# Optimization experiments

Measured on AMD Instinct MI355X. Metric: run time of the kernel, lower is better.

The kernel has to match this reference:

```python
import jax, jax.numpy as jnp
import numpy as np

DIM = 256
HEADS = 8
HEAD_DIM = DIM // HEADS
B = 8
HH, WW = 32, 32
N = HH * WW
TABLE = (2 * HH - 1) * (2 * WW - 1)  # 3969
CPB_HID = 512


def _l2norm(t, eps=1e-12):
    # matches torch F.normalize(dim=-1): x / max(||x||, eps)
    n = jnp.sqrt(jnp.sum(t * t, axis=-1, keepdims=True))
    return t / jnp.maximum(n, eps)


def setup_inputs() -> dict:
    key = jax.random.key(0)
    ks = jax.random.split(key, 12)
    x = jax.random.normal(ks[0], (B, N, DIM), dtype=jnp.float32)
    relative_pos_index = jax.random.randint(ks[1], (N, N), 0, TABLE)
    relative_coords_table = jax.random.normal(ks[2], (TABLE, 2), dtype=jnp.float32)
    s = 0.02
    qkv_w = jax.random.normal(ks[3], (3 * DIM, DIM), dtype=jnp.float32) * s
    qkv_b = jnp.zeros((3 * DIM,), dtype=jnp.float32)
    query_embedding = jax.random.normal(ks[4], (HEADS, 1, HEAD_DIM), dtype=jnp.float32) * s
    # temperature init: log(exp(1/0.24) - 1) so softplus(temperature) = 1/0.24
    temperature = jnp.full((HEADS, 1, 1), float(np.log(np.expm1(1.0 / 0.24))), dtype=jnp.float32)
    proj_w = jax.random.normal(ks[5], (DIM, DIM), dtype=jnp.float32) * s
    proj_b = jnp.zeros((DIM,), dtype=jnp.float32)
    cpb_fc1_w = jax.random.normal(ks[6], (CPB_HID, 2), dtype=jnp.float32) * s
    cpb_fc1_b = jnp.zeros((CPB_HID,), dtype=jnp.float32)
    cpb_fc2_w = jax.random.normal(ks[7], (HEADS, CPB_HID), dtype=jnp.float32) * s
    cpb_fc2_b = jnp.zeros((HEADS,), dtype=jnp.float32)
    return dict(x=x, H=HH, W=WW, relative_pos_index=relative_pos_index,
                relative_coords_table=relative_coords_table,
                qkv_w=qkv_w, qkv_b=qkv_b, query_embedding=query_embedding,
                temperature=temperature, proj_w=proj_w, proj_b=proj_b,
                cpb_fc1_w=cpb_fc1_w, cpb_fc1_b=cpb_fc1_b,
                cpb_fc2_w=cpb_fc2_w, cpb_fc2_b=cpb_fc2_b)


def reference(x, H, W, relative_pos_index, relative_coords_table,
              qkv_w, qkv_b, query_embedding, temperature,
              proj_w, proj_b, cpb_fc1_w, cpb_fc1_b, cpb_fc2_w, cpb_fc2_b):
    Bc, Nc, C = x.shape
    seq_length_scale = jnp.asarray(np.log(HH * WW), dtype=x.dtype)  # from init input_resolution
    # qkv projection -> [B, heads, N, head_dim] each
    qkv = (x @ qkv_w.T + qkv_b).reshape(Bc, Nc, 3 * HEADS, HEAD_DIM).transpose(0, 2, 1, 3)
    q, k, v = qkv[:, :HEADS], qkv[:, HEADS:2 * HEADS], qkv[:, 2 * HEADS:]
    # CPB relative position bias: small MLP over coord table, then NxN gather
    h = jax.nn.relu(relative_coords_table @ cpb_fc1_w.T + cpb_fc1_b)  # [T, 512]
    table = (h @ cpb_fc2_w.T + cpb_fc2_b).T                           # [heads, T]
    rel_bias = table[:, relative_pos_index.reshape(-1)].reshape(HEADS, Nc, Nc)
    # cosine attention with learned temperature
    qn = _l2norm(q) + query_embedding[None]                           # [B, heads, N, hd]
    scale = jax.nn.softplus(temperature) * seq_length_scale           # [heads, 1, 1]
    attn = jnp.einsum('bhnd,bhmd->bhnm', qn * scale[None], _l2norm(k)) + rel_bias[None]
    attn = jax.nn.softmax(attn, axis=-1)
    out = jnp.einsum('bhnm,bhmd->bhnd', attn, v).transpose(0, 2, 1, 3).reshape(Bc, Nc, C)
    return out @ proj_w.T + proj_b
```

## Files before the change

### kernel.cpp

```cpp
#include <hip/hip_runtime.h>
#include <hip/hip_bf16.h>
#include <cstddef>
#include <cstdint>

typedef float v4f __attribute__((ext_vector_type(4)));
typedef short v8s __attribute__((ext_vector_type(8)));
typedef _Float16 v8h __attribute__((ext_vector_type(8)));

__device__ __forceinline__ uint32_t fbits(float x){ uint32_t u; __builtin_memcpy(&u,&x,4); return u; }
__device__ __forceinline__ float ffrom(uint32_t u){ float f; __builtin_memcpy(&f,&u,4); return f; }
__device__ __forceinline__ short bf_rh(float x){ return (short)((fbits(x)+0x8000u)>>16); }
__device__ __forceinline__ uint32_t pack_bf_rh(float a, float b){
    uint32_t ua = fbits(a)+0x8000u, ub = fbits(b)+0x8000u;
#if __has_builtin(__builtin_amdgcn_perm)
    return __builtin_amdgcn_perm(ub, ua, 0x07060302u);
#else
    return (ua>>16) | (ub & 0xFFFF0000u);
#endif
}
__device__ __forceinline__ short f2h(float x){ _Float16 h = (_Float16)x; short s; __builtin_memcpy(&s,&h,2); return s; }
#if __has_builtin(__builtin_amdgcn_exp2f)
#define EXP2(x) __builtin_amdgcn_exp2f(x)
#else
#define EXP2(x) exp2f(x)
#endif

__device__ __forceinline__ void gld16(const void* g, void* l) {
    __builtin_amdgcn_global_load_lds(
        (const __attribute__((address_space(1))) unsigned int*)g,
        (__attribute__((address_space(3))) unsigned int*)l, 16, 0, 0);
}
#define MFMA(a,b,c)  __builtin_amdgcn_mfma_f32_16x16x32_bf16((a),(b),(c),0,0,0)
#define MFMAH(a,b,c) __builtin_amdgcn_mfma_f32_16x16x32_f16((a),(b),(c),0,0,0)

#define LOG2E 1.4426950408889634f

__global__ __launch_bounds__(256)
void fused_qkv(const float* __restrict__ x,   const float* __restrict__ wq,
               const float* __restrict__ wp,  const float* __restrict__ rct,
               const float* __restrict__ fc1w, const float* __restrict__ fc1b,
               const float* __restrict__ fc2w, const float* __restrict__ fc2b,
               const float* __restrict__ qkvb, const float* __restrict__ qe,
               const float* __restrict__ temp, const int* __restrict__ rpi,
               short* __restrict__ qh, short* __restrict__ kh,
               short* __restrict__ vt, float* __restrict__ tblf,
               short* __restrict__ wph, unsigned long long* __restrict__ bi)
{
    __shared__ __align__(16) char smem[49152];
    int bid  = blockIdx.x;
    int tid  = threadIdx.x;
    int w    = tid >> 6;
    int lane = tid & 63;
    int t    = lane & 15;
    int quad = lane >> 4;
    int lr8  = lane >> 3, lc8 = lane & 7;

    if (bid < 63) {
        float* s1 = (float*)smem;
        float* sb = s1 + 1024;
        float* s2 = sb + 512;
        for (int i = tid; i < 1024; i += 256) s1[i] = fc1w[i];
        for (int i = tid; i < 512;  i += 256) sb[i] = fc1b[i];
        for (int i = tid; i < 4096; i += 256) s2[i] = fc2w[i];
        __syncthreads();
        int rl = tid >> 2, jp = tid & 3;
        bool ok = rl < 63;
        int r = bid * 63 + rl;
        float c0 = ok ? rct[2*r]   : 0.f;
        float c1 = ok ? rct[2*r+1] : 0.f;
        float a[8] = {0,0,0,0,0,0,0,0};
        int j0 = jp * 128;
        #pragma unroll 4
        for (int j = j0; j < j0 + 128; ++j) {
            float hv = fmaxf(c0*s1[2*j] + c1*s1[2*j+1] + sb[j], 0.0f);
            #pragma unroll
            for (int hh = 0; hh < 8; ++hh) a[hh] += hv * s2[hh*512 + j];
        }
        #pragma unroll
        for (int hh = 0; hh < 8; ++hh) {
            a[hh] += __shfl_xor(a[hh], 1);
            a[hh] += __shfl_xor(a[hh], 2);
        }
        if (ok && jp == 0) {
            #pragma unroll
            for (int hh = 0; hh < 8; ++hh)
                tblf[hh*3969 + r] = (a[hh] + fc2b[hh]) * LOG2E;
        }
    } else if (bid < 95) {
        int base8 = (bid - 63) * 256;
        int e0 = (base8 + tid) * 8;
        int m  = e0 >> 8;
        int k  = e0 & 255;
        int kt = k >> 6, c = (k >> 3) & 7;
        float4 f0 = *(const float4*)(wp + e0);
        float4 f1 = *(const float4*)(wp + e0 + 4);
        float v[8] = {f0.x,f0.y,f0.z,f0.w,f1.x,f1.y,f1.z,f1.w};
        v8s hi;
        #pragma unroll
        for (int j = 0; j < 8; ++j) hi[j] = f2h(v[j]);
        int dst = m*256 + kt*64 + ((c ^ (m & 7)) << 3);
        *(v8s*)&wph[dst] = hi;
    } else if (bid < 159) {
        int q16 = bid - 95;
        int grp = tid >> 6;
        #pragma unroll 1
        for (int c = 0; c < 16; ++c) {
            int combo = grp*16 + c;
            int kt = combo >> 2, g = combo & 3;
            unsigned long long pk = 0;
            #pragma unroll
            for (int r = 0; r < 4; ++r) {
                int idx = rpi[(size_t)(q16*16 + quad*4 + r)*1024 + kt*64 + 4*t + g];
                pk |= (unsigned long long)(idx & 0xFFFF) << (16*r);
            }
            bi[((size_t)(q16*16 + kt)*4 + g)*64 + lane] = pk;
        }
    } else {
        short* A0 = (short*)smem;
        short* A1 = A0 + 128*64;
        short* W0 = A1 + 128*64;
        short* W1 = W0 + 64*64;
        int g2 = bid - 159;
        int n0 = (g2 % 12) * 64, m0 = (g2 / 12) * 128;
        int Mw = (w >> 1) * 64, Nw = (w & 1) * 32;

        v4f acc[4][2];
        #pragma unroll
        for (int mt = 0; mt < 4; ++mt)
            #pragma unroll
            for (int nt = 0; nt < 2; ++nt) acc[mt][nt] = (v4f){0,0,0,0};

        #pragma unroll 1
        for (int kt2 = 0; kt2 < 2; ++kt2) {
            __syncthreads();
            #pragma unroll
            for (int half = 0; half < 2; ++half) {
                int kt = kt2*2 + half;
                short* Ad = half ? A1 : A0;
                short* Wd = half ? W1 : W0;
                #pragma unroll
                for (int i = 0; i < 4; ++i) {
                    int rr = w*32 + i*8 + lr8;
                    const float* s = x + (size_t)(m0 + rr)*256 + kt*64 + lc8*8;
                    float4 f0 = *(const float4*)s;
                    float4 f1 = *(const float4*)(s + 4);
                    v8h hv;
                    hv[0]=(_Float16)f0.x; hv[1]=(_Float16)f0.y;
                    hv[2]=(_Float16)f0.z; hv[3]=(_Float16)f0.w;
                    hv[4]=(_Float16)f1.x; hv[5]=(_Float16)f1.y;
                    hv[6]=(_Float16)f1.z; hv[7]=(_Float16)f1.w;
                    *(v8h*)&Ad[rr*64 + ((lc8 ^ lr8) << 3)] = hv;
                }
                #pragma unroll
                for (int i = 0; i < 2; ++i) {
                    int rr = w*16 + i*8 + lr8;
                    const float* s = wq + (size_t)(n0 + rr)*256 + kt*64 + lc8*8;
                    float4 f0 = *(const float4*)s;
                    float4 f1 = *(const float4*)(s + 4);
                    v8h hv;
                    hv[0]=(_Float16)f0.x; hv[1]=(_Float16)f0.y;
                    hv[2]=(_Float16)f0.z; hv[3]=(_Float16)f0.w;
                    hv[4]=(_Float16)f1.x; hv[5]=(_Float16)f1.y;
                    hv[6]=(_Float16)f1.z; hv[7]=(_Float16)f1.w;
                    *(v8h*)&Wd[rr*64 + ((lc8 ^ lr8) << 3)] = hv;
                }
            }
            __syncthreads();
            #pragma unroll
            for (int half = 0; half < 2; ++half) {
                const short* As = half ? A1 : A0;
                const short* Ws = half ? W1 : W0;
                #pragma unroll
                for (int kk = 0; kk < 2; ++kk) {
                    int cp = ((kk*4 + quad) ^ (t & 7)) << 3;
                    v8h bh8[2];
                    #pragma unroll
                    for (int nt = 0; nt < 2; ++nt)
                        bh8[nt] = *(const v8h*)&Ws[(Nw + nt*16 + t)*64 + cp];
                    #pragma unroll
                    for (int mt = 0; mt < 4; ++mt) {
                        v8h ah = *(const v8h*)&As[(Mw + mt*16 + t)*64 + cp];
                        #pragma unroll
                        for (int nt = 0; nt < 2; ++nt)
                            acc[mt][nt] = MFMAH(ah, bh8[nt], acc[mt][nt]);
                    }
                }
            }
        }

        #pragma unroll
        for (int nt = 0; nt < 2; ++nt) {
            float bv = qkvb[n0 + Nw + nt*16 + t];
            #pragma unroll
            for (int mt = 0; mt < 4; ++mt)
                #pragma unroll
                for (int r = 0; r < 4; ++r) acc[mt][nt][r] += bv;
        }

        int which = n0 >> 8;
        if (which < 2) {
            int head = ((n0 + Nw) >> 5) & 7;
            float scale = 0.f;
            if (which == 0)
                scale = log1pf(__expf(temp[head])) * 10.0f;
            #pragma unroll
            for (int mt = 0; mt < 4; ++mt)
                #pragma unroll
                for (int r = 0; r < 4; ++r) {
                    float a0 = acc[mt][0][r], a1 = acc[mt][1][r];
                    float s = a0*a0 + a1*a1;
                    s += __shfl_xor(s, 1); s += __shfl_xor(s, 2);
                    s += __shfl_xor(s, 4); s += __shfl_xor(s, 8);
                    float inv = 1.0f / fmaxf(sqrtf(s), 1e-12f);
                    int m = m0 + Mw + mt*16 + quad*4 + r;
                    int b = m >> 10, nrow = m & 1023;
                    if (which == 0) {
                        size_t rowoff = (((size_t)b*8 + head)*1024 + nrow) * 32;
                        #pragma unroll
                        for (int nt = 0; nt < 2; ++nt) {
                            int d = nt*16 + t;
                            float val = (acc[mt][nt][r] * inv + qe[head*32 + d]) * scale;
                            qh[rowoff + d] = f2h(val);
                        }
                    } else {
                        int kk = nrow & 63;
                        int pp = (kk & 3)*16 + (kk >> 2);
                        int prow = (nrow & ~63) | pp;
                        int swk = (kk >> 3) & 3;
                        size_t rowoff = (((size_t)b*8 + head)*1024 + prow) * 32;
                        #pragma unroll
                        for (int nt = 0; nt < 2; ++nt) {
                            int d = nt*16 + t;
                            int dpos = (((d >> 3) ^ swk) << 3) | (d & 7);
                            kh[rowoff + dpos] = f2h(acc[mt][nt][r] * inv);
                        }
                    }
                }
        } else {
            __syncthreads();
            short* VT = (short*)smem;
            #pragma unroll
            for (int mt = 0; mt < 4; ++mt)
                #pragma unroll
                for (int nt = 0; nt < 2; ++nt) {
                    int cl = Nw + nt*16 + t;
                    #pragma unroll
                    for (int r = 0; r < 4; ++r) {
                        int rl = Mw + mt*16 + quad*4 + r;
                        VT[cl*136 + rl] = bf_rh(acc[mt][nt][r]);
                    }
                }
            __syncthreads();
            int b = m0 >> 10;
            int keybase = m0 & 1023;
            int headbase = ((n0 - 512) >> 5) & 7;
            int cl = tid >> 2;
            int dim = cl & 31;
            int hd  = headbase + (cl >> 5);
            size_t obase = (((size_t)b*8 + hd)*32 + dim) * 1024 + keybase;
            #pragma unroll
            for (int pz = 0; pz < 4; ++pz) {
                int ci  = (tid & 3) * 4 + pz;
                int ktl = ci >> 3, c = ci & 7;
                v8s val = *(const v8s*)&VT[cl*136 + ktl*64 + c*8];
                *(v8s*)&vt[obase + ktl*64 + ((c ^ (dim & 7)) << 3)] = val;
            }
        }
    }
}

__global__ __launch_bounds__(512)
void attn_mfma(const short* __restrict__ qh, const short* __restrict__ kh,
               const short* __restrict__ vt,
               const unsigned long long* __restrict__ bi,
               const float* __restrict__ tblf,
               short* __restrict__ yh)
{
    __shared__ __align__(16) short Kh_s[2][2048];
    __shared__ __align__(16) short Vt_s[2][2048];
    __shared__ __align__(16) short Ps[8][16][68];
    __shared__ float tb[3972];

    int bh  = blockIdx.x & 63;
    int qt  = blockIdx.x >> 6;
    int h   = bh & 7;
    int b   = bh >> 3;
    int tid = threadIdx.x;
    int w    = tid >> 6;
    int lane = tid & 63;
    int t    = lane & 15;
    int quad = lane >> 4;

    for (int i = tid; i < 3969; i += 512) tb[i] = tblf[h*3969 + i];

    size_t qoff = ((size_t)bh*1024 + qt*128 + w*16 + t) * 32 + quad*8;
    v8h qf = *(const v8h*)(qh + qoff);

    v4f Oacc[2] = {{0,0,0,0},{0,0,0,0}};
    float lsum[4] = {0,0,0,0};

    size_t kgbase = (size_t)bh * 32768;
    const unsigned long long* bmb = bi + (size_t)(qt*8 + w)*4096 + lane;
    int qrow0 = qt*128 + w*16 + quad*4;
    int swzS = (quad ^ ((t >> 1) & 3)) << 3;
    int lr8 = lane >> 3, lc8 = lane & 7;

    if (w < 4)
        gld16(kh + kgbase + w*512 + lane*8, &Kh_s[0][w*512]);
    else
        gld16(vt + kgbase + (size_t)((w-4)*8 + lr8)*1024 + lc8*8, &Vt_s[0][(w-4)*512]);
    unsigned long long curb[4];
    #pragma unroll
    for (int g = 0; g < 4; ++g) curb[g] = bmb[g*64];

    #pragma unroll 1
    for (int kt = 0; kt < 16; ++kt) {
        int cur = kt & 1;
        __syncthreads();
        unsigned long long nxtb[4];
        if (kt < 15) {
            int nkt = kt + 1, nb = cur ^ 1;
            if (w < 4)
                gld16(kh + kgbase + (size_t)nkt*2048 + w*512 + lane*8, &Kh_s[nb][w*512]);
            else
                gld16(vt + kgbase + (size_t)((w-4)*8 + lr8)*1024 + nkt*64 + lc8*8,
                      &Vt_s[nb][(w-4)*512]);
            #pragma unroll
            for (int g = 0; g < 4; ++g) nxtb[g] = bmb[nkt*256 + g*64];
        }

        v4f S[4];
        #pragma unroll
        for (int g = 0; g < 4; ++g) {
            v8h kb = *(const v8h*)&Kh_s[cur][(g*16 + t)*32 + swzS];
            unsigned long long cb = curb[g];
            v4f c;
            c[0] = tb[(uint32_t)cb & 0xFFFFu];
            c[1] = tb[(uint32_t)(cb >> 16) & 0xFFFFu];
            c[2] = tb[(uint32_t)(cb >> 32) & 0xFFFFu];
            c[3] = tb[(uint32_t)(cb >> 48)];
            S[g] = MFMAH(qf, kb, c);
        }

        #pragma unroll
        for (int r = 0; r < 4; ++r) {
            float p0 = EXP2(S[0][r]);
            float p1 = EXP2(S[1][r]);
            float p2 = EXP2(S[2][r]);
            float p3 = EXP2(S[3][r]);
            lsum[r] += (p0 + p1) + (p2 + p3);
            uint2 pk;
            pk.x = pack_bf_rh(p0, p1);
            pk.y = pack_bf_rh(p2, p3);
            *(uint2*)&Ps[w][quad*4 + r][t*4] = pk;
        }

        #pragma unroll
        for (int ks = 0; ks < 2; ++ks) {
            v8s pf = *(const v8s*)&Ps[w][t][ks*32 + quad*8];
            int vsw = ((ks*4 + quad) ^ (t & 7)) << 3;
            #pragma unroll
            for (int g = 0; g < 2; ++g) {
                v8s vf = *(const v8s*)&Vt_s[cur][(g*16 + t)*64 + vsw];
                Oacc[g] = MFMA(pf, vf, Oacc[g]);
            }
        }
        #pragma unroll
        for (int g = 0; g < 4; ++g) curb[g] = nxtb[g];
    }

    #pragma unroll
    for (int r = 0; r < 4; ++r) {
        float l = lsum[r];
        l += __shfl_xor(l, 1); l += __shfl_xor(l, 2);
        l += __shfl_xor(l, 4); l += __shfl_xor(l, 8);
        float inv = 1.0f / l;
        int qrow = qrow0 + r;
        int m = b*1024 + qrow;
        size_t mbase = (size_t)m * 256;
        int mk = m & 7;
        #pragma unroll
        for (int g = 0; g < 2; ++g) {
            float o = Oacc[g][r] * inv;
            int c = h*4 + g*2 + (t >> 3);
            int chp = ((c ^ mk) << 3) | (t & 7);
            yh[mbase + chp] = f2h(o);
        }
    }
}

__global__ __launch_bounds__(256)
void gemm_proj(const short* __restrict__ Ah_g, const short* __restrict__ Wh_g,
               const float* __restrict__ bias, float* __restrict__ C, int N)
{
    __shared__ __align__(16) short As[2][4096];
    __shared__ __align__(16) short Ws[2][4096];

    int tid  = threadIdx.x;
    int w    = tid >> 6;
    int lane = tid & 63;
    int t    = lane & 15;
    int quad = lane >> 4;
    int m0 = blockIdx.y * 64, n0 = blockIdx.x * 64;
    int Mw = (w >> 1) * 32, Nw = (w & 1) * 32;

    v4f acc[2][2];
    #pragma unroll
    for (int mt = 0; mt < 2; ++mt)
        #pragma unroll
        for (int nt = 0; nt < 2; ++nt) acc[mt][nt] = (v4f){0,0,0,0};

    int lr8 = lane >> 3, lc8 = lane & 7;
    #pragma unroll 1
    for (int kt2 = 0; kt2 < 2; ++kt2) {
        __syncthreads();
        #pragma unroll
        for (int half = 0; half < 2; ++half) {
            int kt = kt2*2 + half;
            #pragma unroll
            for (int i = 0; i < 2; ++i) {
                size_t grow = (size_t)(m0 + w*16 + i*8 + lr8) * 256 + kt*64 + lc8*8;
                gld16(Ah_g + grow, &As[half][(w*16 + i*8) * 64]);
            }
            #pragma unroll
            for (int i = 0; i < 2; ++i) {
                size_t grow = (size_t)(n0 + w*16 + i*8 + lr8) * 256 + kt*64 + lc8*8;
                gld16(Wh_g + grow, &Ws[half][(w*16 + i*8) * 64]);
            }
        }
        __syncthreads();
        #pragma unroll
        for (int half = 0; half < 2; ++half) {
            #pragma unroll
            for (int kk = 0; kk < 2; ++kk) {
                int cp = ((kk*4 + quad) ^ (t & 7)) << 3;
                v8h bh8[2];
                #pragma unroll
                for (int nt = 0; nt < 2; ++nt)
                    bh8[nt] = *(const v8h*)&Ws[half][(Nw + nt*16 + t)*64 + cp];
                #pragma unroll
                for (int mt = 0; mt < 2; ++mt) {
                    v8h ah = *(const v8h*)&As[half][(Mw + mt*16 + t)*64 + cp];
                    #pragma unroll
                    for (int nt = 0; nt < 2; ++nt)
                        acc[mt][nt] = MFMAH(ah, bh8[nt], acc[mt][nt]);
                }
            }
        }
    }

    #pragma unroll
    for (int nt = 0; nt < 2; ++nt) {
        float bv = bias[n0 + Nw + nt*16 + t];
        #pragma unroll
        for (int mt = 0; mt < 2; ++mt)
            #pragma unroll
            for (int r = 0; r < 4; ++r) acc[mt][nt][r] += bv;
    }
    #pragma unroll
    for (int mt = 0; mt < 2; ++mt)
        #pragma unroll
        for (int r = 0; r < 4; ++r) {
            int m = m0 + Mw + mt*16 + quad*4 + r;
            #pragma unroll
            for (int nt = 0; nt < 2; ++nt)
                C[(size_t)m * N + n0 + Nw + nt*16 + t] = acc[mt][nt][r];
        }
}

extern "C" void kernel_launch(void* const* d_in, const int* in_sizes, int n_in,
                              void* d_out, int out_size, void* d_ws, size_t ws_size,
                              hipStream_t stream)
{
    const float* x     = (const float*)d_in[0];
    const int*   rpi   = (const int*)d_in[3];
    const float* rct   = (const float*)d_in[4];
    const float* qkvw  = (const float*)d_in[5];
    const float* qkvb  = (const float*)d_in[6];
    const float* qe    = (const float*)d_in[7];
    const float* temp  = (const float*)d_in[8];
    const float* projw = (const float*)d_in[9];
    const float* projb = (const float*)d_in[10];
    const float* fc1w  = (const float*)d_in[11];
    const float* fc1b  = (const float*)d_in[12];
    const float* fc2w  = (const float*)d_in[13];
    const float* fc2b  = (const float*)d_in[14];

    char* p = (char*)d_ws;
    float* tblf  = (float*)p;  p += 131072;
    short* y     = (short*)p;  p += 4194304;
    short* wph   = (short*)p;  p += 131072;
    short* qh    = (short*)p;  p += 4194304;
    short* kh    = (short*)p;  p += 4194304;
    short* vt    = (short*)p;  p += 4194304;
    unsigned long long* bi = (unsigned long long*)p; p += 2097152;
    float* out   = (float*)d_out;

    fused_qkv<<<927, 256, 0, stream>>>(x, qkvw, projw, rct,
                                       fc1w, fc1b, fc2w, fc2b,
                                       qkvb, qe, temp, rpi,
                                       qh, kh, vt, tblf, wph, bi);

    attn_mfma<<<512, 512, 0, stream>>>(qh, kh, vt, bi, tblf, y);

    dim3 g2(256/64, 8192/64);
    gemm_proj<<<g2, 256, 0, stream>>>(y, wph, projb, out, 256);
}
```

Baseline: 148.4 us.

## Fuse output projection into attention kernel via last-arriving-block atomic counter

Removes the separate projection GEMM launch. Blocks are reordered so that the eight heads sharing a (batch, query-tile) row group increment a per-group atomic counter. The last block to finish then runs the 128x256 projection for that group from the fp16 attention output, using the shared memory that attention already used. This saves a kernel launch and its tail, but the projection is serialized onto one block per group, which lowers its parallelism and adds fences and atomics. The counters are reset inside the first kernel.

```diff
diff --git a/kernel.cpp b/kernel.cpp
--- a/kernel.cpp
+++ b/kernel.cpp
@@ -44,7 +44,8 @@
                const float* __restrict__ temp, const int* __restrict__ rpi,
                short* __restrict__ qh, short* __restrict__ kh,
                short* __restrict__ vt, float* __restrict__ tblf,
-               short* __restrict__ wph, unsigned long long* __restrict__ bi)
+               short* __restrict__ wph, unsigned long long* __restrict__ bi,
+               unsigned* __restrict__ done)
 {
     __shared__ __align__(16) char smem[49152];
     int bid  = blockIdx.x;
@@ -102,6 +103,7 @@
         *(v8s*)&wph[dst] = hi;
     } else if (bid < 159) {
         int q16 = bid - 95;
+        if (q16 == 0 && tid < 64) done[tid] = 0;
         int grp = tid >> 6;
         #pragma unroll 1
         for (int c = 0; c < 16; ++c) {
@@ -274,22 +276,30 @@
                const short* __restrict__ vt,
                const unsigned long long* __restrict__ bi,
                const float* __restrict__ tblf,
-               short* __restrict__ yh)
+               short* __restrict__ yh,
+               const short* __restrict__ wph,
+               const float* __restrict__ projb,
+               float* __restrict__ out,
+               unsigned* __restrict__ done)
 {
-    __shared__ __align__(16) short Kh_s[2][2048];
-    __shared__ __align__(16) short Vt_s[2][2048];
-    __shared__ __align__(16) short Ps[8][16][68];
-    __shared__ float tb[3972];
-
-    int bh  = blockIdx.x & 63;
-    int qt  = blockIdx.x >> 6;
-    int h   = bh & 7;
-    int b   = bh >> 3;
+    __shared__ __align__(16) char smem[49696];
+    __shared__ unsigned wflag;
+    short* Kh  = (short*)smem;
+    short* Vts = Kh + 4096;
+    short* Psb = Vts + 4096;
+    float* tb  = (float*)(Psb + 8704);
+
+    int h   = blockIdx.x >> 6;
+    int g   = blockIdx.x & 63;
+    int b   = g >> 3;
+    int qt  = g & 7;
+    int bh  = b*8 + h;
     int tid = threadIdx.x;
     int w    = tid >> 6;
     int lane = tid & 63;
     int t    = lane & 15;
     int quad = lane >> 4;
+    int lr8 = lane >> 3, lc8 = lane & 7;
 
     for (int i = tid; i < 3969; i += 512) tb[i] = tblf[h*3969 + i];
 
@@ -303,15 +313,14 @@
     const unsigned long long* bmb = bi + (size_t)(qt*8 + w)*4096 + lane;
     int qrow0 = qt*128 + w*16 + quad*4;
     int swzS = (quad ^ ((t >> 1) & 3)) << 3;
-    int lr8 = lane >> 3, lc8 = lane & 7;
 
     if (w < 4)
-        gld16(kh + kgbase + w*512 + lane*8, &Kh_s[0][w*512]);
+        gld16(kh + kgbase + w*512 + lane*8, &Kh[w*512]);
     else
-        gld16(vt + kgbase + (size_t)((w-4)*8 + lr8)*1024 + lc8*8, &Vt_s[0][(w-4)*512]);
+        gld16(vt + kgbase + (size_t)((w-4)*8 + lr8)*1024 + lc8*8, &Vts[(w-4)*512]);
     unsigned long long curb[4];
     #pragma unroll
-    for (int g = 0; g < 4; ++g) curb[g] = bmb[g*64];
+    for (int gg = 0; gg < 4; ++gg) curb[gg] = bmb[gg*64];
 
     #pragma unroll 1
     for (int kt = 0; kt < 16; ++kt) {
@@ -321,25 +330,26 @@
         if (kt < 15) {
             int nkt = kt + 1, nb = cur ^ 1;
             if (w < 4)
-                gld16(kh + kgbase + (size_t)nkt*2048 + w*512 + lane*8, &Kh_s[nb][w*512]);
+                gld16(kh + kgbase + (size_t)nkt*2048 + w*512 + lane*8,
+                      &Kh[nb*2048 + w*512]);
             else
                 gld16(vt + kgbase + (size_t)((w-4)*8 + lr8)*1024 + nkt*64 + lc8*8,
-                      &Vt_s[nb][(w-4)*512]);
-            #pragma unroll
-            for (int g = 0; g < 4; ++g) nxtb[g] = bmb[nkt*256 + g*64];
+                      &Vts[nb*2048 + (w-4)*512]);
+            #pragma unroll
+            for (int gg = 0; gg < 4; ++gg) nxtb[gg] = bmb[nkt*256 + gg*64];
         }
 
         v4f S[4];
         #pragma unroll
-        for (int g = 0; g < 4; ++g) {
-            v8h kb = *(const v8h*)&Kh_s[cur][(g*16 + t)*32 + swzS];
-            unsigned long long cb = curb[g];
+        for (int gg = 0; gg < 4; ++gg) {
+            v8h kb = *(const v8h*)&Kh[cur*2048 + (gg*16 + t)*32 + swzS];
+            unsigned long long cb = curb[gg];
             v4f c;
             c[0] = tb[(uint32_t)cb & 0xFFFFu];
             c[1] = tb[(uint32_t)(cb >> 16) & 0xFFFFu];
             c[2] = tb[(uint32_t)(cb >> 32) & 0xFFFFu];
             c[3] = tb[(uint32_t)(cb >> 48)];
-            S[g] = MFMAH(qf, kb, c);
+            S[gg] = MFMAH(qf, kb, c);
         }
 
         #pragma unroll
@@ -352,21 +362,21 @@
             uint2 pk;
             pk.x = pack_bf_rh(p0, p1);
             pk.y = pack_bf_rh(p2, p3);
-            *(uint2*)&Ps[w][quad*4 + r][t*4] = pk;
+            *(uint2*)&Psb[(w*16 + quad*4 + r)*68 + t*4] = pk;
         }
 
         #pragma unroll
         for (int ks = 0; ks < 2; ++ks) {
-            v8s pf = *(const v8s*)&Ps[w][t][ks*32 + quad*8];
+            v8s pf = *(const v8s*)&Psb[(w*16 + t)*68 + ks*32 + quad*8];
             int vsw = ((ks*4 + quad) ^ (t & 7)) << 3;
             #pragma unroll
-            for (int g = 0; g < 2; ++g) {
-                v8s vf = *(const v8s*)&Vt_s[cur][(g*16 + t)*64 + vsw];
-                Oacc[g] = MFMA(pf, vf, Oacc[g]);
-            }
-        }
-        #pragma unroll
-        for (int g = 0; g < 4; ++g) curb[g] = nxtb[g];
+            for (int gg = 0; gg < 2; ++gg) {
+                v8s vf = *(const v8s*)&Vts[cur*2048 + (gg*16 + t)*64 + vsw];
+                Oacc[gg] = MFMA(pf, vf, Oacc[gg]);
+            }
+        }
+        #pragma unroll
+        for (int gg = 0; gg < 4; ++gg) curb[gg] = nxtb[gg];
     }
 
     #pragma unroll
@@ -380,92 +390,93 @@
         size_t mbase = (size_t)m * 256;
         int mk = m & 7;
         #pragma unroll
-        for (int g = 0; g < 2; ++g) {
-            float o = Oacc[g][r] * inv;
-            int c = h*4 + g*2 + (t >> 3);
+        for (int gg = 0; gg < 2; ++gg) {
+            float o = Oacc[gg][r] * inv;
+            int c = h*4 + gg*2 + (t >> 3);
             int chp = ((c ^ mk) << 3) | (t & 7);
             yh[mbase + chp] = f2h(o);
         }
     }
-}
-
-__global__ __launch_bounds__(256)
-void gemm_proj(const short* __restrict__ Ah_g, const short* __restrict__ Wh_g,
-               const float* __restrict__ bias, float* __restrict__ C, int N)
-{
-    __shared__ __align__(16) short As[2][4096];
-    __shared__ __align__(16) short Ws[2][4096];
-
-    int tid  = threadIdx.x;
-    int w    = tid >> 6;
-    int lane = tid & 63;
-    int t    = lane & 15;
-    int quad = lane >> 4;
-    int m0 = blockIdx.y * 64, n0 = blockIdx.x * 64;
-    int Mw = (w >> 1) * 32, Nw = (w & 1) * 32;
-
-    v4f acc[2][2];
-    #pragma unroll
-    for (int mt = 0; mt < 2; ++mt)
-        #pragma unroll
-        for (int nt = 0; nt < 2; ++nt) acc[mt][nt] = (v4f){0,0,0,0};
-
-    int lr8 = lane >> 3, lc8 = lane & 7;
+
+    __threadfence();
+    __syncthreads();
+    if (tid == 0) {
+        unsigned prev = __hip_atomic_fetch_add(&done[g], 1u,
+                            __ATOMIC_ACQ_REL, __HIP_MEMORY_SCOPE_AGENT);
+        wflag = (prev == 7u);
+    }
+    __syncthreads();
+    if (!wflag) return;
+    __threadfence();
+    __syncthreads();
+
+    int m0g = b*1024 + qt*128;
+    int grp = w >> 2;
+    int wl  = w & 3;
+    short* Asg = (short*)smem + grp*8192;
+    short* Wsg = Asg + 4096;
+    int Mw = (wl >> 1) * 32, Nw = (wl & 1) * 32;
+
     #pragma unroll 1
-    for (int kt2 = 0; kt2 < 2; ++kt2) {
-        __syncthreads();
-        #pragma unroll
-        for (int half = 0; half < 2; ++half) {
-            int kt = kt2*2 + half;
+    for (int vbp = 0; vbp < 4; ++vbp) {
+        int v = vbp*2 + grp;
+        int m0v = m0g + (v >> 2) * 64;
+        int n0v = (v & 3) * 64;
+        v4f pacc[2][2];
+        #pragma unroll
+        for (int mt = 0; mt < 2; ++mt)
+            #pragma unroll
+            for (int nt = 0; nt < 2; ++nt) pacc[mt][nt] = (v4f){0,0,0,0};
+
+        #pragma unroll 1
+        for (int kt3 = 0; kt3 < 4; ++kt3) {
+            __syncthreads();
             #pragma unroll
             for (int i = 0; i < 2; ++i) {
-                size_t grow = (size_t)(m0 + w*16 + i*8 + lr8) * 256 + kt*64 + lc8*8;
-                gld16(Ah_g + grow, &As[half][(w*16 + i*8) * 64]);
+                int rr = wl*16 + i*8 + lr8;
+                gld16(yh + (size_t)(m0v + rr)*256 + kt3*64 + lc8*8, Asg + rr*64);
             }
             #pragma unroll
             for (int i = 0; i < 2; ++i) {
-                size_t grow = (size_t)(n0 + w*16 + i*8 + lr8) * 256 + kt*64 + lc8*8;
-                gld16(Wh_g + grow, &Ws[half][(w*16 + i*8) * 64]);
-            }
-        }
-        __syncthreads();
-        #pragma unroll
-        for (int half = 0; half < 2; ++half) {
+                int rr = wl*16 + i*8 + lr8;
+                gld16(wph + (size_t)(n0v + rr)*256 + kt3*64 + lc8*8, Wsg + rr*64);
+            }
+            __syncthreads();
             #pragma unroll
             for (int kk = 0; kk < 2; ++kk) {
                 int cp = ((kk*4 + quad) ^ (t & 7)) << 3;
                 v8h bh8[2];
                 #pragma unroll
                 for (int nt = 0; nt < 2; ++nt)
-                    bh8[nt] = *(const v8h*)&Ws[half][(Nw + nt*16 + t)*64 + cp];
+                    bh8[nt] = *(const v8h*)&Wsg[(Nw + nt*16 + t)*64 + cp];
                 #pragma unroll
                 for (int mt = 0; mt < 2; ++mt) {
-                    v8h ah = *(const v8h*)&As[half][(Mw + mt*16 + t)*64 + cp];
+                    v8h ah = *(const v8h*)&Asg[(Mw + mt*16 + t)*64 + cp];
                     #pragma unroll
                     for (int nt = 0; nt < 2; ++nt)
-                        acc[mt][nt] = MFMAH(ah, bh8[nt], acc[mt][nt]);
+                        pacc[mt][nt] = MFMAH(ah, bh8[nt], pacc[mt][nt]);
                 }
             }
         }
+
+        #pragma unroll
+        for (int nt = 0; nt < 2; ++nt) {
+            float bv = projb[n0v + Nw + nt*16 + t];
+            #pragma unroll
+            for (int mt = 0; mt < 2; ++mt)
+                #pragma unroll
+                for (int r = 0; r < 4; ++r) pacc[mt][nt][r] += bv;
+        }
+        #pragma unroll
+        for (int mt = 0; mt < 2; ++mt)
+            #pragma unroll
+            for (int r = 0; r < 4; ++r) {
+                int m = m0v + Mw + mt*16 + quad*4 + r;
+                #pragma unroll
+                for (int nt = 0; nt < 2; ++nt)
+                    out[(size_t)m * 256 + n0v + Nw + nt*16 + t] = pacc[mt][nt][r];
+            }
     }
-
-    #pragma unroll
-    for (int nt = 0; nt < 2; ++nt) {
-        float bv = bias[n0 + Nw + nt*16 + t];
-        #pragma unroll
-        for (int mt = 0; mt < 2; ++mt)
-            #pragma unroll
-            for (int r = 0; r < 4; ++r) acc[mt][nt][r] += bv;
-    }
-    #pragma unroll
-    for (int mt = 0; mt < 2; ++mt)
-        #pragma unroll
-        for (int r = 0; r < 4; ++r) {
-            int m = m0 + Mw + mt*16 + quad*4 + r;
-            #pragma unroll
-            for (int nt = 0; nt < 2; ++nt)
-                C[(size_t)m * N + n0 + Nw + nt*16 + t] = acc[mt][nt][r];
-        }
 }
 
 extern "C" void kernel_launch(void* const* d_in, const int* in_sizes, int n_in,
@@ -494,15 +505,14 @@
     short* kh    = (short*)p;  p += 4194304;
     short* vt    = (short*)p;  p += 4194304;
     unsigned long long* bi = (unsigned long long*)p; p += 2097152;
+    unsigned* done = (unsigned*)p; p += 256;
     float* out   = (float*)d_out;
 
     fused_qkv<<<927, 256, 0, stream>>>(x, qkvw, projw, rct,
                                        fc1w, fc1b, fc2w, fc2b,
                                        qkvb, qe, temp, rpi,
-                                       qh, kh, vt, tblf, wph, bi);
-
-    attn_mfma<<<512, 512, 0, stream>>>(qh, kh, vt, bi, tblf, y);
-
-    dim3 g2(256/64, 8192/64);
-    gemm_proj<<<g2, 256, 0, stream>>>(y, wph, projb, out, 256);
+                                       qh, kh, vt, tblf, wph, bi, done);
+
+    attn_mfma<<<512, 512, 0, stream>>>(qh, kh, vt, bi, tblf, y,
+                                       wph, projb, out, done);
 }
```

Result: slower. 283.6 us (+91.1%).

## Shrink attention blocks to 64 queries and gather bias from global memory

Applied to the files above, without the earlier changes.

The attention kernel now uses 256-thread blocks covering 64 query rows, launched as 1024 blocks instead of 512. The per-head bias table is no longer staged into shared memory; each lane gathers its bias values straight from global memory (through cache), one key tile ahead, as part of the prefetch. This removes the ~16KB per-block table fill and cuts LDS use, which should allow more resident blocks. In exchange, K/V tiles are reloaded for twice as many blocks, and each lane issues scattered global gathers that hold more registers.

```diff
diff --git a/kernel.cpp b/kernel.cpp
--- a/kernel.cpp
+++ b/kernel.cpp
@@ -269,20 +269,19 @@
     }
 }
 
-__global__ __launch_bounds__(512)
+__global__ __launch_bounds__(256)
 void attn_mfma(const short* __restrict__ qh, const short* __restrict__ kh,
                const short* __restrict__ vt,
                const unsigned long long* __restrict__ bi,
                const float* __restrict__ tblf,
                short* __restrict__ yh)
 {
-    __shared__ __align__(16) short Kh_s[2][2048];
-    __shared__ __align__(16) short Vt_s[2][2048];
-    __shared__ __align__(16) short Ps[8][16][68];
-    __shared__ float tb[3972];
+    __shared__ __align__(16) short Kh[2][2048];
+    __shared__ __align__(16) short Vts[2][2048];
+    __shared__ __align__(16) short Psb[4*16*68];
 
     int bh  = blockIdx.x & 63;
-    int qt  = blockIdx.x >> 6;
+    int qt2 = blockIdx.x >> 6;
     int h   = bh & 7;
     int b   = bh >> 3;
     int tid = threadIdx.x;
@@ -290,56 +289,72 @@
     int lane = tid & 63;
     int t    = lane & 15;
     int quad = lane >> 4;
-
-    for (int i = tid; i < 3969; i += 512) tb[i] = tblf[h*3969 + i];
-
-    size_t qoff = ((size_t)bh*1024 + qt*128 + w*16 + t) * 32 + quad*8;
+    int lr8 = lane >> 3, lc8 = lane & 7;
+
+    size_t qoff = ((size_t)bh*1024 + qt2*64 + w*16 + t) * 32 + quad*8;
     v8h qf = *(const v8h*)(qh + qoff);
 
     v4f Oacc[2] = {{0,0,0,0},{0,0,0,0}};
     float lsum[4] = {0,0,0,0};
 
     size_t kgbase = (size_t)bh * 32768;
-    const unsigned long long* bmb = bi + (size_t)(qt*8 + w)*4096 + lane;
-    int qrow0 = qt*128 + w*16 + quad*4;
+    const unsigned long long* bmb = bi + (size_t)(qt2*4 + w)*4096 + lane;
+    const float* tbg = tblf + h*3969;
+    int qrow0 = qt2*64 + w*16 + quad*4;
     int swzS = (quad ^ ((t >> 1) & 3)) << 3;
-    int lr8 = lane >> 3, lc8 = lane & 7;
-
-    if (w < 4)
-        gld16(kh + kgbase + w*512 + lane*8, &Kh_s[0][w*512]);
-    else
-        gld16(vt + kgbase + (size_t)((w-4)*8 + lr8)*1024 + lc8*8, &Vt_s[0][(w-4)*512]);
-    unsigned long long curb[4];
+
+    if (w < 2) {
+        gld16(kh + kgbase + (w*2+0)*512 + lane*8, &Kh[0][(w*2+0)*512]);
+        gld16(kh + kgbase + (w*2+1)*512 + lane*8, &Kh[0][(w*2+1)*512]);
+    } else {
+        int v0 = w - 2;
+        gld16(vt + kgbase + (size_t)(v0*16 + lr8)*1024 + lc8*8,     &Vts[0][(v0*2+0)*512]);
+        gld16(vt + kgbase + (size_t)(v0*16 + 8 + lr8)*1024 + lc8*8, &Vts[0][(v0*2+1)*512]);
+    }
+    v4f curc[4];
     #pragma unroll
-    for (int g = 0; g < 4; ++g) curb[g] = bmb[g*64];
+    for (int g = 0; g < 4; ++g) {
+        unsigned long long cb = bmb[g*64];
+        curc[g][0] = tbg[(uint32_t)cb & 0xFFFFu];
+        curc[g][1] = tbg[(uint32_t)(cb >> 16) & 0xFFFFu];
+        curc[g][2] = tbg[(uint32_t)(cb >> 32) & 0xFFFFu];
+        curc[g][3] = tbg[(uint32_t)(cb >> 48)];
+    }
 
     #pragma unroll 1
     for (int kt = 0; kt < 16; ++kt) {
         int cur = kt & 1;
         __syncthreads();
-        unsigned long long nxtb[4];
+        v4f nxtc[4];
         if (kt < 15) {
             int nkt = kt + 1, nb = cur ^ 1;
-            if (w < 4)
-                gld16(kh + kgbase + (size_t)nkt*2048 + w*512 + lane*8, &Kh_s[nb][w*512]);
-            else
-                gld16(vt + kgbase + (size_t)((w-4)*8 + lr8)*1024 + nkt*64 + lc8*8,
-                      &Vt_s[nb][(w-4)*512]);
-            #pragma unroll
-            for (int g = 0; g < 4; ++g) nxtb[g] = bmb[nkt*256 + g*64];
+            if (w < 2) {
+                gld16(kh + kgbase + (size_t)nkt*2048 + (w*2+0)*512 + lane*8,
+                      &Kh[nb][(w*2+0)*512]);
+                gld16(kh + kgbase + (size_t)nkt*2048 + (w*2+1)*512 + lane*8,
+                      &Kh[nb][(w*2+1)*512]);
+            } else {
+                int v0 = w - 2;
+                gld16(vt + kgbase + (size_t)(v0*16 + lr8)*1024 + nkt*64 + lc8*8,
+                      &Vts[nb][(v0*2+0)*512]);
+                gld16(vt + kgbase + (size_t)(v0*16 + 8 + lr8)*1024 + nkt*64 + lc8*8,
+                      &Vts[nb][(v0*2+1)*512]);
+            }
+            #pragma unroll
+            for (int g = 0; g < 4; ++g) {
+                unsigned long long cb = bmb[nkt*256 + g*64];
+                nxtc[g][0] = tbg[(uint32_t)cb & 0xFFFFu];
+                nxtc[g][1] = tbg[(uint32_t)(cb >> 16) & 0xFFFFu];
+                nxtc[g][2] = tbg[(uint32_t)(cb >> 32) & 0xFFFFu];
+                nxtc[g][3] = tbg[(uint32_t)(cb >> 48)];
+            }
         }
 
         v4f S[4];
         #pragma unroll
         for (int g = 0; g < 4; ++g) {
-            v8h kb = *(const v8h*)&Kh_s[cur][(g*16 + t)*32 + swzS];
-            unsigned long long cb = curb[g];
-            v4f c;
-            c[0] = tb[(uint32_t)cb & 0xFFFFu];
-            c[1] = tb[(uint32_t)(cb >> 16) & 0xFFFFu];
-            c[2] = tb[(uint32_t)(cb >> 32) & 0xFFFFu];
-            c[3] = tb[(uint32_t)(cb >> 48)];
-            S[g] = MFMAH(qf, kb, c);
+            v8h kb = *(const v8h*)&Kh[cur][(g*16 + t)*32 + swzS];
+            S[g] = MFMAH(qf, kb, curc[g]);
         }
 
         #pragma unroll
@@ -352,21 +367,21 @@
             uint2 pk;
             pk.x = pack_bf_rh(p0, p1);
             pk.y = pack_bf_rh(p2, p3);
-            *(uint2*)&Ps[w][quad*4 + r][t*4] = pk;
+            *(uint2*)&Psb[(w*16 + quad*4 + r)*68 + t*4] = pk;
         }
 
         #pragma unroll
         for (int ks = 0; ks < 2; ++ks) {
-            v8s pf = *(const v8s*)&Ps[w][t][ks*32 + quad*8];
+            v8s pf = *(const v8s*)&Psb[(w*16 + t)*68 + ks*32 + quad*8];
             int vsw = ((ks*4 + quad) ^ (t & 7)) << 3;
             #pragma unroll
             for (int g = 0; g < 2; ++g) {
-                v8s vf = *(const v8s*)&Vt_s[cur][(g*16 + t)*64 + vsw];
+                v8s vf = *(const v8s*)&Vts[cur][(g*16 + t)*64 + vsw];
                 Oacc[g] = MFMA(pf, vf, Oacc[g]);
             }
         }
         #pragma unroll
-        for (int g = 0; g < 4; ++g) curb[g] = nxtb[g];
+        for (int g = 0; g < 4; ++g) curc[g] = nxtc[g];
     }
 
     #pragma unroll
@@ -501,7 +516,7 @@
                                        qkvb, qe, temp, rpi,
                                        qh, kh, vt, tblf, wph, bi);
 
-    attn_mfma<<<512, 512, 0, stream>>>(qh, kh, vt, bi, tblf, y);
+    attn_mfma<<<1024, 256, 0, stream>>>(qh, kh, vt, bi, tblf, y);
 
     dim3 g2(256/64, 8192/64);
     gemm_proj<<<g2, 256, 0, stream>>>(y, wph, projb, out, 256);
```

After: 204.0 us. 1.37x slower.
